# Kernel optimization log

Measured on AMD Instinct MI355X. Metric: run time of the kernel, lower is better.

Reference implementation:

```python
import jax, jax.numpy as jnp
import numpy as np

N = 100000
E = 1600000
F_IN, F_HID, F_OUT = 128, 64, 1


def setup_inputs() -> dict:
    key = jax.random.key(0)
    ks = jax.random.split(key, 8)
    x = jax.random.normal(ks[0], (N, F_IN), dtype=jnp.float32)
    edge_index = jax.random.randint(ks[1], (2, E), 0, N, dtype=jnp.int64)
    def glorot(k, fan_in, fan_out):
        scale = jnp.sqrt(2.0 / (fan_in + fan_out)).astype(jnp.float32)
        return jax.random.normal(k, (fan_in, fan_out), dtype=jnp.float32) * scale
    W1 = glorot(ks[2], F_IN, F_HID); b1 = jnp.zeros((F_HID,), jnp.float32)
    W2 = glorot(ks[3], F_HID, F_HID); b2 = jnp.zeros((F_HID,), jnp.float32)
    W3 = glorot(ks[4], F_HID, F_OUT); b3 = jnp.zeros((F_OUT,), jnp.float32)
    return {"x": x, "W1": W1, "b1": b1, "W2": W2, "b2": b2, "W3": W3, "b3": b3, "edge_index": edge_index}


def _gcn_norm(edge_index, n):
    # add self-loops, symmetric D^{-1/2} (A+I) D^{-1/2} normalization (PyG GCNConv default)
    loop = jnp.arange(n, dtype=edge_index.dtype)
    src = jnp.concatenate([edge_index[0], loop])
    dst = jnp.concatenate([edge_index[1], loop])
    deg = jax.ops.segment_sum(jnp.ones_like(src, dtype=jnp.float32), dst, num_segments=n)
    dis = jnp.where(deg > 0, jax.lax.rsqrt(jnp.maximum(deg, 1.0)), 0.0)
    norm = dis[src] * dis[dst]  # [E+N]
    return src, dst, norm


def _gcn_conv(h, W, b, src, dst, norm, n):
    h = h @ W                                   # [N, f_out]
    msg = h[src] * norm[:, None]                # gather + scale, [E+N, f_out]
    out = jax.ops.segment_sum(msg, dst, num_segments=n)  # scatter-add
    return out + b


def reference(x, W1, b1, W2, b2, W3, b3, edge_index):
    n = x.shape[0]
    src, dst, norm = _gcn_norm(edge_index, n)
    h = jax.nn.relu(_gcn_conv(x, W1, b1, src, dst, norm, n))
    h = jax.nn.relu(_gcn_conv(h, W2, b2, src, dst, norm, n))
    h = _gcn_conv(h, W3, b3, src, dst, norm, n)
    return jax.nn.sigmoid(h)
```

## Files before the change

kernel.cpp:

```cpp
#include <hip/hip_runtime.h>
#include <math.h>

#define NN 100000
#define NE 1600000
#define NSHARD 4
#define SHARD_W (NN / NSHARD)
#define NCHUNK 64
#define CHUNK_E (NE / NCHUNK)
#define CHUNK_I4 (CHUNK_E / 4)

typedef __attribute__((ext_vector_type(8))) short bf16x8;
typedef __attribute__((ext_vector_type(4))) float f32x4;
typedef __attribute__((ext_vector_type(2))) float f32x2;

__device__ inline unsigned f2bf(float f) {
    unsigned u = __float_as_uint(f);
    u += 0x7FFFu + ((u >> 16) & 1u);
    return u >> 16;
}
__device__ inline float bflo(unsigned v) { return __uint_as_float(v << 16); }
__device__ inline float bfhi(unsigned v) { return __uint_as_float(v & 0xFFFF0000u); }
__device__ inline f32x2 bfpair(unsigned u) {
    f32x2 r;
    r.x = __uint_as_float(u << 16);
    r.y = __uint_as_float(u & 0xFFFF0000u);
    return r;
}

__global__ __launch_bounds__(256) void k_cnt(const int4* __restrict__ dst4,
                                             unsigned char* __restrict__ cnt,
                                             unsigned char* __restrict__ lrank) {
    __shared__ __align__(16) unsigned ldeg[SHARD_W];
    int t = threadIdx.x;
    int shard = blockIdx.x & (NSHARD - 1);
    int b = blockIdx.x >> 2;
    int lo = shard * SHARD_W;
    uint4 z4 = make_uint4(0u, 0u, 0u, 0u);
    for (int i = t; i < SHARD_W / 4; i += 256) ((uint4*)ldeg)[i] = z4;
    __syncthreads();
    const int4* p = dst4 + b * CHUNK_I4;
    unsigned char* lr = lrank + b * CHUNK_E;
#pragma unroll 4
    for (int j = t; j < CHUNK_I4; j += 256) {
        int4 d = p[j];
        unsigned ex = (unsigned)(d.x - lo);
        unsigned ey = (unsigned)(d.y - lo);
        unsigned ez = (unsigned)(d.z - lo);
        unsigned ew = (unsigned)(d.w - lo);
        if (ex < SHARD_W) lr[4 * j + 0] = (unsigned char)atomicAdd(&ldeg[ex], 1u);
        if (ey < SHARD_W) lr[4 * j + 1] = (unsigned char)atomicAdd(&ldeg[ey], 1u);
        if (ez < SHARD_W) lr[4 * j + 2] = (unsigned char)atomicAdd(&ldeg[ez], 1u);
        if (ew < SHARD_W) lr[4 * j + 3] = (unsigned char)atomicAdd(&ldeg[ew], 1u);
    }
    __syncthreads();
    unsigned* cb32 = (unsigned*)cnt + b * (NN / 4) + shard * (SHARD_W / 4);
    for (int i = t; i < SHARD_W / 4; i += 256) {
        uint4 v = *(const uint4*)&ldeg[4 * i];
        cb32[i] = (v.x & 255u) | ((v.y & 255u) << 8) | ((v.z & 255u) << 16)
                | ((v.w & 255u) << 24);
    }
}

__global__ __launch_bounds__(256) void k_blkscan(unsigned char* __restrict__ cnt,
                                                 int* __restrict__ deg,
                                                 int* __restrict__ bsums) {
    __shared__ int s[256];
    int i = blockIdx.x * 256 + threadIdx.x;
    int total = 0;
    if (i < NN) {
        unsigned a = 0;
#pragma unroll
        for (int b = 0; b < NCHUNK; ++b) {
            unsigned v = cnt[b * NN + i];
            cnt[b * NN + i] = (unsigned char)a;
            a += v;
        }
        deg[i] = (int)a;
        total = (int)a;
    }
    s[threadIdx.x] = total;
    __syncthreads();
    for (int off = 128; off > 0; off >>= 1) {
        if (threadIdx.x < off) s[threadIdx.x] += s[threadIdx.x + off];
        __syncthreads();
    }
    if (threadIdx.x == 0) bsums[blockIdx.x] = s[0];
}

__global__ void k_rowptr(const int* __restrict__ deg, const int* __restrict__ bsums,
                         int* __restrict__ rowptr, float* __restrict__ dis) {
    __shared__ int sbase[256];
    __shared__ int s[256];
    int t = threadIdx.x;
    int bid = blockIdx.x;
    int v = (t < bid) ? bsums[t] : 0;
    if (t + 256 < bid) v += bsums[t + 256];
    sbase[t] = v;
    __syncthreads();
    for (int off = 128; off > 0; off >>= 1) {
        if (t < off) sbase[t] += sbase[t + off];
        __syncthreads();
    }
    int base = sbase[0];
    int i = bid * 256 + t;
    int d = (i < NN) ? deg[i] : 0;
    s[t] = d;
    __syncthreads();
    for (int off = 1; off < 256; off <<= 1) {
        int x = (t >= off) ? s[t - off] : 0;
        __syncthreads();
        s[t] += x;
        __syncthreads();
    }
    if (i < NN) {
        rowptr[i] = base + s[t] - d;
        dis[i] = rsqrtf((float)(d + 1));
    }
    if (i == 0) rowptr[NN] = NE;
}

__global__ __launch_bounds__(256) void k_build_csr(
    const int4* __restrict__ src4, const int4* __restrict__ dst4,
    const unsigned char* __restrict__ blkoff, const unsigned* __restrict__ lr4,
    const int* __restrict__ rowptr, int* __restrict__ csr) {
    int shard = blockIdx.x & (NSHARD - 1);
    int bsh = blockIdx.x >> 2;
    int stride = (gridDim.x >> 2) * 256;
    int lo = shard * SHARD_W;
    const int NE4 = NE / 4;
    for (int i = bsh * 256 + threadIdx.x; i < NE4; i += stride) {
        int4 d = dst4[i];
        int4 s = src4[i];
        unsigned lr = lr4[i];
        const unsigned char* off = blkoff + (i / CHUNK_I4) * NN;
        unsigned ex = (unsigned)(d.x - lo);
        unsigned ey = (unsigned)(d.y - lo);
        unsigned ez = (unsigned)(d.z - lo);
        unsigned ew = (unsigned)(d.w - lo);
        if (ex < SHARD_W) csr[rowptr[d.x] + off[d.x] + (lr & 255u)] = s.x;
        if (ey < SHARD_W) csr[rowptr[d.y] + off[d.y] + ((lr >> 8) & 255u)] = s.y;
        if (ez < SHARD_W) csr[rowptr[d.z] + off[d.z] + ((lr >> 16) & 255u)] = s.z;
        if (ew < SHARD_W) csr[rowptr[d.w] + off[d.w] + (lr >> 24)] = s.w;
    }
}

#define XS_LD 136
__global__ __launch_bounds__(256) void k_gemm1(
    const float* __restrict__ x, const float* __restrict__ W,
    const float* __restrict__ dis, unsigned short* __restrict__ tsb) {
    __shared__ unsigned short xs[64 * XS_LD];
    __shared__ unsigned short wt[64 * XS_LD];
    int t = threadIdx.x;
    int row0 = blockIdx.x * 64;
    for (int i = t; i < 64 * 64; i += 256) {
        int n = i & 63, k2 = i >> 6;
        float w0 = W[(2 * k2) * 64 + n];
        float w1 = W[(2 * k2 + 1) * 64 + n];
        *(unsigned*)&wt[n * XS_LD + 2 * k2] = f2bf(w0) | (f2bf(w1) << 16);
    }
    for (int i = t; i < 64 * 32; i += 256) {
        int r = i >> 5, c4 = i & 31;
        int gr = row0 + r;
        uint2 p = {0u, 0u};
        if (gr < NN) {
            float4 v = *(const float4*)&x[gr * 128 + 4 * c4];
            p.x = f2bf(v.x) | (f2bf(v.y) << 16);
            p.y = f2bf(v.z) | (f2bf(v.w) << 16);
        }
        *(uint2*)&xs[r * XS_LD + 4 * c4] = p;
    }
    __syncthreads();
    int w = t >> 6, l = t & 63;
    int lm = l & 15, lg = l >> 4;
    const unsigned short* ap = &xs[(16 * w + lm) * XS_LD + 8 * lg];
    const unsigned short* bp = &wt[lm * XS_LD + 8 * lg];
    f32x4 acc0 = {0, 0, 0, 0}, acc1 = {0, 0, 0, 0}, acc2 = {0, 0, 0, 0}, acc3 = {0, 0, 0, 0};
#pragma unroll
    for (int kb = 0; kb < 4; ++kb) {
        bf16x8 a  = *(const bf16x8*)(ap + 32 * kb);
        bf16x8 b0 = *(const bf16x8*)(bp + 32 * kb);
        bf16x8 b1 = *(const bf16x8*)(bp + 16 * XS_LD + 32 * kb);
        bf16x8 b2 = *(const bf16x8*)(bp + 32 * XS_LD + 32 * kb);
        bf16x8 b3 = *(const bf16x8*)(bp + 48 * XS_LD + 32 * kb);
        acc0 = __builtin_amdgcn_mfma_f32_16x16x32_bf16(a, b0, acc0, 0, 0, 0);
        acc1 = __builtin_amdgcn_mfma_f32_16x16x32_bf16(a, b1, acc1, 0, 0, 0);
        acc2 = __builtin_amdgcn_mfma_f32_16x16x32_bf16(a, b2, acc2, 0, 0, 0);
        acc3 = __builtin_amdgcn_mfma_f32_16x16x32_bf16(a, b3, acc3, 0, 0, 0);
    }
    int rbase = row0 + 16 * w + 4 * lg;
#pragma unroll
    for (int r = 0; r < 4; ++r) {
        int row = rbase + r;
        if (row < NN) {
            float dv = dis[row];
            unsigned short* o = &tsb[row * 64 + lm];
            o[0]  = (unsigned short)f2bf(acc0[r] * dv);
            o[16] = (unsigned short)f2bf(acc1[r] * dv);
            o[32] = (unsigned short)f2bf(acc2[r] * dv);
            o[48] = (unsigned short)f2bf(acc3[r] * dv);
        }
    }
}

#define HS_LD 72
__global__ __launch_bounds__(256) void k_gemm2(
    const unsigned short* __restrict__ hb, const float* __restrict__ W,
    const float* __restrict__ dis, unsigned short* __restrict__ tsb) {
    __shared__ unsigned short hs[64 * HS_LD];
    __shared__ unsigned short wh[64 * HS_LD];
    __shared__ unsigned short wl[64 * HS_LD];
    int t = threadIdx.x;
    int row0 = blockIdx.x * 64;
    for (int i = t; i < 64 * 32; i += 256) {
        int n = i & 63, k2 = i >> 6;
        float w0 = W[(2 * k2) * 64 + n];
        float w1 = W[(2 * k2 + 1) * 64 + n];
        unsigned h0 = f2bf(w0), h1 = f2bf(w1);
        *(unsigned*)&wh[n * HS_LD + 2 * k2] = h0 | (h1 << 16);
        float r0 = w0 - bflo(h0), r1 = w1 - bflo(h1);
        *(unsigned*)&wl[n * HS_LD + 2 * k2] = f2bf(r0) | (f2bf(r1) << 16);
    }
    const uint4* h4 = (const uint4*)hb;
    for (int i = t; i < 64 * 8; i += 256) {
        int r = i >> 3, c8 = i & 7;
        int gr = row0 + r;
        uint4 v = (gr < NN) ? h4[gr * 8 + c8] : make_uint4(0u, 0u, 0u, 0u);
        *(uint4*)&hs[r * HS_LD + 8 * c8] = v;
    }
    __syncthreads();
    int w = t >> 6, l = t & 63;
    int lm = l & 15, lg = l >> 4;
    const unsigned short* ap = &hs[(16 * w + lm) * HS_LD + 8 * lg];
    const unsigned short* bh = &wh[lm * HS_LD + 8 * lg];
    const unsigned short* bl = &wl[lm * HS_LD + 8 * lg];
    f32x4 acc0 = {0, 0, 0, 0}, acc1 = {0, 0, 0, 0}, acc2 = {0, 0, 0, 0}, acc3 = {0, 0, 0, 0};
#pragma unroll
    for (int kb = 0; kb < 2; ++kb) {
        bf16x8 a  = *(const bf16x8*)(ap + 32 * kb);
        bf16x8 h0 = *(const bf16x8*)(bh + 32 * kb);
        bf16x8 h1 = *(const bf16x8*)(bh + 16 * HS_LD + 32 * kb);
        bf16x8 h2 = *(const bf16x8*)(bh + 32 * HS_LD + 32 * kb);
        bf16x8 h3 = *(const bf16x8*)(bh + 48 * HS_LD + 32 * kb);
        bf16x8 l0 = *(const bf16x8*)(bl + 32 * kb);
        bf16x8 l1 = *(const bf16x8*)(bl + 16 * HS_LD + 32 * kb);
        bf16x8 l2 = *(const bf16x8*)(bl + 32 * HS_LD + 32 * kb);
        bf16x8 l3 = *(const bf16x8*)(bl + 48 * HS_LD + 32 * kb);
        acc0 = __builtin_amdgcn_mfma_f32_16x16x32_bf16(a, h0, acc0, 0, 0, 0);
        acc1 = __builtin_amdgcn_mfma_f32_16x16x32_bf16(a, h1, acc1, 0, 0, 0);
        acc2 = __builtin_amdgcn_mfma_f32_16x16x32_bf16(a, h2, acc2, 0, 0, 0);
        acc3 = __builtin_amdgcn_mfma_f32_16x16x32_bf16(a, h3, acc3, 0, 0, 0);
        acc0 = __builtin_amdgcn_mfma_f32_16x16x32_bf16(a, l0, acc0, 0, 0, 0);
        acc1 = __builtin_amdgcn_mfma_f32_16x16x32_bf16(a, l1, acc1, 0, 0, 0);
        acc2 = __builtin_amdgcn_mfma_f32_16x16x32_bf16(a, l2, acc2, 0, 0, 0);
        acc3 = __builtin_amdgcn_mfma_f32_16x16x32_bf16(a, l3, acc3, 0, 0, 0);
    }
    int rbase = row0 + 16 * w + 4 * lg;
#pragma unroll
    for (int r = 0; r < 4; ++r) {
        int row = rbase + r;
        if (row < NN) {
            float dv = dis[row];
            unsigned short* o = &tsb[row * 64 + lm];
            o[0]  = (unsigned short)f2bf(acc0[r] * dv);
            o[16] = (unsigned short)f2bf(acc1[r] * dv);
            o[32] = (unsigned short)f2bf(acc2[r] * dv);
            o[48] = (unsigned short)f2bf(acc3[r] * dv);
        }
    }
}

#define AGG_BLOCKS 2048
template <bool FUSE3>
__global__ __launch_bounds__(256) void k_agg_relu(
    const unsigned short* __restrict__ tsb, const int* __restrict__ rowptr,
    const int* __restrict__ csr, const float* __restrict__ dis,
    const float* __restrict__ b, const float* __restrict__ W3,
    unsigned short* __restrict__ hb, float* __restrict__ t3) {
    int wid = blockIdx.x * 4 + (threadIdx.x >> 6);
    const int nwaves = AGG_BLOCKS * 4;
    int lane = threadIdx.x & 63;
    int half = lane >> 5;
    int oct = (lane >> 3) & 3;
    int fl = lane & 7;
    const uint4* ts128 = (const uint4*)tsb;
    for (int base = wid * 2; base < NN; base += nwaves * 2) {
        int node = base + half;
        bool valid = node < NN;
        f32x2 a0 = {0.f, 0.f}, a1 = {0.f, 0.f}, a2 = {0.f, 0.f}, a3 = {0.f, 0.f};
        if (valid) {
            if (oct == 0) {
                uint4 v = ts128[node * 8 + fl];
                a0 += bfpair(v.x); a1 += bfpair(v.y); a2 += bfpair(v.z); a3 += bfpair(v.w);
            }
            int e = rowptr[node] + oct, end = rowptr[node + 1];
            for (; e + 12 < end; e += 16) {
                int s0 = csr[e];
                int s1 = csr[e + 4];
                int s2 = csr[e + 8];
                int s3 = csr[e + 12];
                uint4 v0 = ts128[s0 * 8 + fl];
                uint4 v1 = ts128[s1 * 8 + fl];
                uint4 v2 = ts128[s2 * 8 + fl];
                uint4 v3 = ts128[s3 * 8 + fl];
                a0 += bfpair(v0.x); a1 += bfpair(v0.y); a2 += bfpair(v0.z); a3 += bfpair(v0.w);
                a0 += bfpair(v1.x); a1 += bfpair(v1.y); a2 += bfpair(v1.z); a3 += bfpair(v1.w);
                a0 += bfpair(v2.x); a1 += bfpair(v2.y); a2 += bfpair(v2.z); a3 += bfpair(v2.w);
                a0 += bfpair(v3.x); a1 += bfpair(v3.y); a2 += bfpair(v3.z); a3 += bfpair(v3.w);
            }
            for (; e < end; e += 4) {
                uint4 v = ts128[csr[e] * 8 + fl];
                a0 += bfpair(v.x); a1 += bfpair(v.y); a2 += bfpair(v.z); a3 += bfpair(v.w);
            }
        }
#pragma unroll
        for (int off = 8; off <= 16; off <<= 1) {
            a0.x += __shfl_xor(a0.x, off); a0.y += __shfl_xor(a0.y, off);
            a1.x += __shfl_xor(a1.x, off); a1.y += __shfl_xor(a1.y, off);
            a2.x += __shfl_xor(a2.x, off); a2.y += __shfl_xor(a2.y, off);
            a3.x += __shfl_xor(a3.x, off); a3.y += __shfl_xor(a3.y, off);
        }
        if (valid && oct == 0) {
            float dv = dis[node];
            float v0 = fmaxf(a0.x * dv + b[8 * fl + 0], 0.f);
            float v1 = fmaxf(a0.y * dv + b[8 * fl + 1], 0.f);
            float v2 = fmaxf(a1.x * dv + b[8 * fl + 2], 0.f);
            float v3 = fmaxf(a1.y * dv + b[8 * fl + 3], 0.f);
            float v4 = fmaxf(a2.x * dv + b[8 * fl + 4], 0.f);
            float v5 = fmaxf(a2.y * dv + b[8 * fl + 5], 0.f);
            float v6 = fmaxf(a3.x * dv + b[8 * fl + 6], 0.f);
            float v7 = fmaxf(a3.y * dv + b[8 * fl + 7], 0.f);
            if (FUSE3) {
                float part = v0 * W3[8 * fl + 0] + v1 * W3[8 * fl + 1]
                           + v2 * W3[8 * fl + 2] + v3 * W3[8 * fl + 3]
                           + v4 * W3[8 * fl + 4] + v5 * W3[8 * fl + 5]
                           + v6 * W3[8 * fl + 6] + v7 * W3[8 * fl + 7];
                part += __shfl_xor(part, 1);
                part += __shfl_xor(part, 2);
                part += __shfl_xor(part, 4);
                if (fl == 0) t3[node] = part * dv;
            } else {
                uint4 p;
                p.x = f2bf(v0) | (f2bf(v1) << 16);
                p.y = f2bf(v2) | (f2bf(v3) << 16);
                p.z = f2bf(v4) | (f2bf(v5) << 16);
                p.w = f2bf(v6) | (f2bf(v7) << 16);
                ((uint4*)hb)[node * 8 + fl] = p;
            }
        }
    }
}

__global__ void k_out(const float* __restrict__ t3, const int* __restrict__ rowptr,
                      const int* __restrict__ csr, const float* __restrict__ dis,
                      const float* __restrict__ b3, float* __restrict__ out) {
    int wv = blockIdx.x * 4 + (threadIdx.x >> 6);
    int lane = threadIdx.x & 63;
    int g = lane >> 3;
    int sl = lane & 7;
    int node = wv * 8 + g;
    if (node >= NN) return;
    float acc = (sl == 0) ? t3[node] : 0.f;
    float acc1 = 0.f;
    int e = rowptr[node] + sl, end = rowptr[node + 1];
    for (; e + 8 < end; e += 16) {
        acc += t3[csr[e]];
        acc1 += t3[csr[e + 8]];
    }
    if (e < end) acc += t3[csr[e]];
    acc += acc1;
    acc += __shfl_xor(acc, 1);
    acc += __shfl_xor(acc, 2);
    acc += __shfl_xor(acc, 4);
    if (sl == 0) {
        float z = acc * dis[node] + b3[0];
        out[node] = 1.f / (1.f + __expf(-z));
    }
}

extern "C" void kernel_launch(void* const* d_in, const int* in_sizes, int n_in,
                              void* d_out, int out_size, void* d_ws, size_t ws_size,
                              hipStream_t stream) {
    const float* x  = (const float*)d_in[0];
    const float* W1 = (const float*)d_in[1];
    const float* b1 = (const float*)d_in[2];
    const float* W2 = (const float*)d_in[3];
    const float* b2 = (const float*)d_in[4];
    const float* W3 = (const float*)d_in[5];
    const float* b3 = (const float*)d_in[6];
    const int*   ei = (const int*)d_in[7];
    const int* src = ei;
    const int* dst = ei + NE;
    float* out = (float*)d_out;

    unsigned short* TSB = (unsigned short*)d_ws;
    unsigned short* HB  = TSB + (size_t)NN * 64;
    float* dis    = (float*)(HB + (size_t)NN * 64);
    float* t3     = dis + NN;
    int*   deg    = (int*)(t3 + NN);
    int*   rowptr = deg + NN;
    int*   bsums  = rowptr + NN + 8;
    int*   csr    = bsums + 512;
    unsigned char* lrank = (unsigned char*)TSB;
    unsigned char* cnt   = (unsigned char*)HB;

    const int nbN = (NN + 255) / 256;
    const int nbG = (NN + 63) / 64;
    const int nbOut = (NN + 31) / 32;

    k_cnt<<<NSHARD * NCHUNK, 256, 0, stream>>>((const int4*)dst, cnt, lrank);
    k_blkscan<<<nbN, 256, 0, stream>>>(cnt, deg, bsums);
    k_rowptr<<<nbN, 256, 0, stream>>>(deg, bsums, rowptr, dis);
    k_build_csr<<<2048, 256, 0, stream>>>((const int4*)src, (const int4*)dst,
                                          cnt, (const unsigned*)lrank, rowptr, csr);

    k_gemm1<<<nbG, 256, 0, stream>>>(x, W1, dis, TSB);
    k_agg_relu<false><<<AGG_BLOCKS, 256, 0, stream>>>(TSB, rowptr, csr, dis, b1, W3, HB, t3);

    k_gemm2<<<nbG, 256, 0, stream>>>(HB, W2, dis, TSB);

    k_agg_relu<true><<<AGG_BLOCKS, 256, 0, stream>>>(TSB, rowptr, csr, dis, b2, W3, HB, t3);

    k_out<<<nbOut, 256, 0, stream>>>(t3, rowptr, csr, dis, b3, out);
}
```

Before: 264.5 us.

## Fuse layer-2 GEMM into first aggregation epilogue using shared-memory weights

Removes the separate k_gemm2 MFMA kernel. The first aggregation kernel now loads W2 into shared memory, multiplies each node's relu output by W2 with FP32 FMAs using lane shuffles, and writes the dis-scaled bf16 result directly. This saves one launch and one full write and read of the N×64 hidden tensor. In exchange the aggregation epilogue does 64×64 scalar FMAs per node on only 8 active lanes per half-wave, plus a 16KB shared-memory load per block, which may lower occupancy.

```diff
diff --git a/kernel.cpp b/kernel.cpp
--- a/kernel.cpp
+++ b/kernel.cpp
@@ -202,80 +202,18 @@
     }
 }
 
-#define HS_LD 72
-__global__ __launch_bounds__(256) void k_gemm2(
-    const unsigned short* __restrict__ hb, const float* __restrict__ W,
-    const float* __restrict__ dis, unsigned short* __restrict__ tsb) {
-    __shared__ unsigned short hs[64 * HS_LD];
-    __shared__ unsigned short wh[64 * HS_LD];
-    __shared__ unsigned short wl[64 * HS_LD];
-    int t = threadIdx.x;
-    int row0 = blockIdx.x * 64;
-    for (int i = t; i < 64 * 32; i += 256) {
-        int n = i & 63, k2 = i >> 6;
-        float w0 = W[(2 * k2) * 64 + n];
-        float w1 = W[(2 * k2 + 1) * 64 + n];
-        unsigned h0 = f2bf(w0), h1 = f2bf(w1);
-        *(unsigned*)&wh[n * HS_LD + 2 * k2] = h0 | (h1 << 16);
-        float r0 = w0 - bflo(h0), r1 = w1 - bflo(h1);
-        *(unsigned*)&wl[n * HS_LD + 2 * k2] = f2bf(r0) | (f2bf(r1) << 16);
-    }
-    const uint4* h4 = (const uint4*)hb;
-    for (int i = t; i < 64 * 8; i += 256) {
-        int r = i >> 3, c8 = i & 7;
-        int gr = row0 + r;
-        uint4 v = (gr < NN) ? h4[gr * 8 + c8] : make_uint4(0u, 0u, 0u, 0u);
-        *(uint4*)&hs[r * HS_LD + 8 * c8] = v;
-    }
-    __syncthreads();
-    int w = t >> 6, l = t & 63;
-    int lm = l & 15, lg = l >> 4;
-    const unsigned short* ap = &hs[(16 * w + lm) * HS_LD + 8 * lg];
-    const unsigned short* bh = &wh[lm * HS_LD + 8 * lg];
-    const unsigned short* bl = &wl[lm * HS_LD + 8 * lg];
-    f32x4 acc0 = {0, 0, 0, 0}, acc1 = {0, 0, 0, 0}, acc2 = {0, 0, 0, 0}, acc3 = {0, 0, 0, 0};
-#pragma unroll
-    for (int kb = 0; kb < 2; ++kb) {
-        bf16x8 a  = *(const bf16x8*)(ap + 32 * kb);
-        bf16x8 h0 = *(const bf16x8*)(bh + 32 * kb);
-        bf16x8 h1 = *(const bf16x8*)(bh + 16 * HS_LD + 32 * kb);
-        bf16x8 h2 = *(const bf16x8*)(bh + 32 * HS_LD + 32 * kb);
-        bf16x8 h3 = *(const bf16x8*)(bh + 48 * HS_LD + 32 * kb);
-        bf16x8 l0 = *(const bf16x8*)(bl + 32 * kb);
-        bf16x8 l1 = *(const bf16x8*)(bl + 16 * HS_LD + 32 * kb);
-        bf16x8 l2 = *(const bf16x8*)(bl + 32 * HS_LD + 32 * kb);
-        bf16x8 l3 = *(const bf16x8*)(bl + 48 * HS_LD + 32 * kb);
-        acc0 = __builtin_amdgcn_mfma_f32_16x16x32_bf16(a, h0, acc0, 0, 0, 0);
-        acc1 = __builtin_amdgcn_mfma_f32_16x16x32_bf16(a, h1, acc1, 0, 0, 0);
-        acc2 = __builtin_amdgcn_mfma_f32_16x16x32_bf16(a, h2, acc2, 0, 0, 0);
-        acc3 = __builtin_amdgcn_mfma_f32_16x16x32_bf16(a, h3, acc3, 0, 0, 0);
-        acc0 = __builtin_amdgcn_mfma_f32_16x16x32_bf16(a, l0, acc0, 0, 0, 0);
-        acc1 = __builtin_amdgcn_mfma_f32_16x16x32_bf16(a, l1, acc1, 0, 0, 0);
-        acc2 = __builtin_amdgcn_mfma_f32_16x16x32_bf16(a, l2, acc2, 0, 0, 0);
-        acc3 = __builtin_amdgcn_mfma_f32_16x16x32_bf16(a, l3, acc3, 0, 0, 0);
-    }
-    int rbase = row0 + 16 * w + 4 * lg;
-#pragma unroll
-    for (int r = 0; r < 4; ++r) {
-        int row = rbase + r;
-        if (row < NN) {
-            float dv = dis[row];
-            unsigned short* o = &tsb[row * 64 + lm];
-            o[0]  = (unsigned short)f2bf(acc0[r] * dv);
-            o[16] = (unsigned short)f2bf(acc1[r] * dv);
-            o[32] = (unsigned short)f2bf(acc2[r] * dv);
-            o[48] = (unsigned short)f2bf(acc3[r] * dv);
-        }
-    }
-}
-
 #define AGG_BLOCKS 2048
-template <bool FUSE3>
+template <int MODE>
 __global__ __launch_bounds__(256) void k_agg_relu(
     const unsigned short* __restrict__ tsb, const int* __restrict__ rowptr,
     const int* __restrict__ csr, const float* __restrict__ dis,
-    const float* __restrict__ b, const float* __restrict__ W3,
-    unsigned short* __restrict__ hb, float* __restrict__ t3) {
+    const float* __restrict__ b, const float* __restrict__ Wx,
+    unsigned short* __restrict__ outb, float* __restrict__ t3) {
+    __shared__ float Ws[(MODE == 1) ? 64 * 64 : 1];
+    if (MODE == 1) {
+        for (int i = threadIdx.x; i < 64 * 64; i += 256) Ws[i] = Wx[i];
+        __syncthreads();
+    }
     int wid = blockIdx.x * 4 + (threadIdx.x >> 6);
     const int nwaves = AGG_BLOCKS * 4;
     int lane = threadIdx.x & 63;
@@ -319,8 +257,8 @@
             a2.x += __shfl_xor(a2.x, off); a2.y += __shfl_xor(a2.y, off);
             a3.x += __shfl_xor(a3.x, off); a3.y += __shfl_xor(a3.y, off);
         }
-        if (valid && oct == 0) {
-            float dv = dis[node];
+        if (oct == 0) {
+            float dv = valid ? dis[node] : 0.f;
             float v0 = fmaxf(a0.x * dv + b[8 * fl + 0], 0.f);
             float v1 = fmaxf(a0.y * dv + b[8 * fl + 1], 0.f);
             float v2 = fmaxf(a1.x * dv + b[8 * fl + 2], 0.f);
@@ -329,22 +267,50 @@
             float v5 = fmaxf(a2.y * dv + b[8 * fl + 5], 0.f);
             float v6 = fmaxf(a3.x * dv + b[8 * fl + 6], 0.f);
             float v7 = fmaxf(a3.y * dv + b[8 * fl + 7], 0.f);
-            if (FUSE3) {
-                float part = v0 * W3[8 * fl + 0] + v1 * W3[8 * fl + 1]
-                           + v2 * W3[8 * fl + 2] + v3 * W3[8 * fl + 3]
-                           + v4 * W3[8 * fl + 4] + v5 * W3[8 * fl + 5]
-                           + v6 * W3[8 * fl + 6] + v7 * W3[8 * fl + 7];
+            if (MODE == 1) {
+                float hv[8] = {v0, v1, v2, v3, v4, v5, v6, v7};
+                float c0 = 0.f, c1 = 0.f, c2 = 0.f, c3 = 0.f;
+                float c4 = 0.f, c5 = 0.f, c6 = 0.f, c7 = 0.f;
+                int sbase = half << 5;
+#pragma unroll
+                for (int kr = 0; kr < 8; ++kr) {
+                    float hs = hv[kr];
+#pragma unroll
+                    for (int kf = 0; kf < 8; ++kf) {
+                        float hk = __shfl(hs, sbase + kf, 64);
+                        const float* wr = &Ws[(kf * 8 + kr) * 64 + 8 * fl];
+                        float4 wa = *(const float4*)wr;
+                        float4 wb = *(const float4*)(wr + 4);
+                        c0 += hk * wa.x; c1 += hk * wa.y;
+                        c2 += hk * wa.z; c3 += hk * wa.w;
+                        c4 += hk * wb.x; c5 += hk * wb.y;
+                        c6 += hk * wb.z; c7 += hk * wb.w;
+                    }
+                }
+                if (valid) {
+                    uint4 p;
+                    p.x = f2bf(c0 * dv) | (f2bf(c1 * dv) << 16);
+                    p.y = f2bf(c2 * dv) | (f2bf(c3 * dv) << 16);
+                    p.z = f2bf(c4 * dv) | (f2bf(c5 * dv) << 16);
+                    p.w = f2bf(c6 * dv) | (f2bf(c7 * dv) << 16);
+                    ((uint4*)outb)[node * 8 + fl] = p;
+                }
+            } else if (MODE == 2) {
+                float part = v0 * Wx[8 * fl + 0] + v1 * Wx[8 * fl + 1]
+                           + v2 * Wx[8 * fl + 2] + v3 * Wx[8 * fl + 3]
+                           + v4 * Wx[8 * fl + 4] + v5 * Wx[8 * fl + 5]
+                           + v6 * Wx[8 * fl + 6] + v7 * Wx[8 * fl + 7];
                 part += __shfl_xor(part, 1);
                 part += __shfl_xor(part, 2);
                 part += __shfl_xor(part, 4);
-                if (fl == 0) t3[node] = part * dv;
-            } else {
+                if (valid && fl == 0) t3[node] = part * dv;
+            } else if (valid) {
                 uint4 p;
                 p.x = f2bf(v0) | (f2bf(v1) << 16);
                 p.y = f2bf(v2) | (f2bf(v3) << 16);
                 p.z = f2bf(v4) | (f2bf(v5) << 16);
                 p.w = f2bf(v6) | (f2bf(v7) << 16);
-                ((uint4*)hb)[node * 8 + fl] = p;
+                ((uint4*)outb)[node * 8 + fl] = p;
             }
         }
     }
@@ -414,11 +380,10 @@
                                           cnt, (const unsigned*)lrank, rowptr, csr);
 
     k_gemm1<<<nbG, 256, 0, stream>>>(x, W1, dis, TSB);
-    k_agg_relu<false><<<AGG_BLOCKS, 256, 0, stream>>>(TSB, rowptr, csr, dis, b1, W3, HB, t3);
-
-    k_gemm2<<<nbG, 256, 0, stream>>>(HB, W2, dis, TSB);
-
-    k_agg_relu<true><<<AGG_BLOCKS, 256, 0, stream>>>(TSB, rowptr, csr, dis, b2, W3, HB, t3);
+
+    k_agg_relu<1><<<AGG_BLOCKS, 256, 0, stream>>>(TSB, rowptr, csr, dis, b1, W2, HB, t3);
+
+    k_agg_relu<2><<<AGG_BLOCKS, 256, 0, stream>>>(HB, rowptr, csr, dis, b2, W3, TSB, t3);
 
     k_out<<<nbOut, 256, 0, stream>>>(t3, rowptr, csr, dis, b3, out);
 }
```

After: 516.2 us. 95.1% more time.
